# Optimization experiments

Measured on AMD Instinct MI355X. Metric: run time of the kernel, lower is better.

## Reference

```python
import jax, jax.numpy as jnp
import numpy as np

B, TK, H = 32, 1024, 512
N = 2 * H          # hidden_dim * 2
AD = 512           # attention_dimension


def setup_inputs() -> dict:
    key = jax.random.key(0)
    ks = jax.random.split(key, 11)
    s = 0.02  # weight scale
    return {
        's_t_hat': jax.random.normal(ks[0], (B, N), jnp.float32),
        'encoder_outputs': jax.random.normal(ks[1], (B, TK, N), jnp.float32),
        'encoder_feature': jax.random.normal(ks[2], (B * TK, N), jnp.float32),
        'enc_padding_mask': jax.random.uniform(ks[3], (B, TK), jnp.float32),
        'coverage': jax.random.uniform(ks[4], (B, TK), jnp.float32),
        'r_i': jax.random.normal(ks[5], (B, TK, AD), jnp.float32),
        'W_s_w': jax.random.normal(ks[6], (N, N), jnp.float32) * s,
        'W_s_b': jax.random.normal(ks[7], (N,), jnp.float32) * s,
        'W_c_w': jax.random.normal(ks[8], (N, 1), jnp.float32) * s,
        'v_w': jax.random.normal(ks[9], (1, N), jnp.float32) * s,
        'W_r_w': jax.random.normal(ks[10], (N, AD), jnp.float32) * s,
    }


def reference(s_t_hat, encoder_outputs, encoder_feature, enc_padding_mask,
              coverage, r_i, W_s_w, W_s_b, W_c_w, v_w, W_r_w):
    b, t_k, n = encoder_outputs.shape
    # decoder feature: W_s(s_t_hat), broadcast over time
    dec_fea = s_t_hat @ W_s_w.T + W_s_b                       # [b, n]
    enc_feat = encoder_feature.reshape(b, t_k, n)             # [b, t_k, n]
    # coverage feature: W_c applied to scalar coverage per position
    cov_feat = coverage[..., None] * W_c_w[:, 0]              # [b, t_k, n]
    e = jnp.tanh(enc_feat + dec_fea[:, None, :] + cov_feat)   # [b, t_k, n]
    scores = jnp.einsum('btn,n->bt', e, v_w[0])               # [b, t_k]
    attn_ = jax.nn.softmax(scores, axis=1) * enc_padding_mask
    attn = attn_ / attn_.sum(1, keepdims=True)                # renormalized
    c_t = jnp.einsum('bt,btn->bn', attn, encoder_outputs)     # [b, n]
    coverage_new = coverage + attn                            # [b, t_k]
    # structural (LSA) branch
    Wrri = jnp.einsum('bta,na->btn', r_i, W_r_w)              # [b, t_k, n]
    e_s = jnp.tanh(Wrri + dec_fea[:, None, :])
    s2 = jnp.einsum('btn,n->bt', e_s, v_w[0])
    a_struct = (jax.nn.softmax(s2, axis=1) * enc_padding_mask)[:, None, :]  # [b,1,t_k]
    c_t_struct = jnp.einsum('bt,btn->bn', a_struct[:, 0], encoder_outputs)  # [b, n]
    return (c_t, attn, coverage_new, c_t_struct, a_struct)
```

## Files before the change

### kernel.cpp

```cpp
#include <hip/hip_runtime.h>
#include <hip/hip_bf16.h>

static constexpr int BB   = 32;
static constexpr int TKK  = 1024;
static constexpr int ND   = 1024;
static constexpr int ADIM = 512;

typedef __attribute__((ext_vector_type(8))) short bf16x8;
typedef __attribute__((ext_vector_type(4))) float f32x4;

__device__ __forceinline__ float fast_tanh(float x) {
  x = fminf(fmaxf(x, -15.f), 15.f);
  float e = __expf(2.f * x);
  return __fdividef(e - 1.f, e + 1.f);
}

__device__ __forceinline__ short f2bf(float x) {
  unsigned u = __float_as_uint(x);
  u += 0x7FFF + ((u >> 16) & 1);
  return (short)(u >> 16);
}

__device__ __forceinline__ void gload_lds16(const void* g, void* l) {
  __builtin_amdgcn_global_load_lds(
      (const __attribute__((address_space(1))) unsigned int*)g,
      (__attribute__((address_space(3))) unsigned int*)l, 16, 0, 0);
}

__global__ __launch_bounds__(256) void k_cvt(const float* __restrict__ src,
    short* __restrict__ dst) {
  size_t i = (size_t)blockIdx.x * 256 + threadIdx.x;
  float4 a = ((const float4*)src)[2 * i];
  float4 b = ((const float4*)src)[2 * i + 1];
  bf16x8 h;
  h[0] = f2bf(a.x); h[1] = f2bf(a.y); h[2] = f2bf(a.z); h[3] = f2bf(a.w);
  h[4] = f2bf(b.x); h[5] = f2bf(b.y); h[6] = f2bf(b.z); h[7] = f2bf(b.w);
  ((bf16x8*)dst)[i] = h;
}

__global__ __launch_bounds__(256) void k_decfea(const float* __restrict__ s_t_hat,
    const float* __restrict__ Wsw, const float* __restrict__ Wsb,
    float* __restrict__ dec) {
  int b  = blockIdx.x >> 3;
  int n0 = (blockIdx.x & 7) << 7;
  int w = threadIdx.x >> 6, lane = threadIdx.x & 63;
  const float4* s4 = (const float4*)(s_t_hat + (size_t)b * ND);
  float4 sv0 = s4[lane], sv1 = s4[lane + 64], sv2 = s4[lane + 128], sv3 = s4[lane + 192];
  for (int nn = 0; nn < 32; nn++) {
    int n = n0 + w * 32 + nn;
    const float4* w4 = (const float4*)(Wsw + (size_t)n * ND);
    float4 wa = w4[lane], wb = w4[lane + 64], wc = w4[lane + 128], wd = w4[lane + 192];
    float acc = sv0.x*wa.x + sv0.y*wa.y + sv0.z*wa.z + sv0.w*wa.w
              + sv1.x*wb.x + sv1.y*wb.y + sv1.z*wb.z + sv1.w*wb.w
              + sv2.x*wc.x + sv2.y*wc.y + sv2.z*wc.z + sv2.w*wc.w
              + sv3.x*wd.x + sv3.y*wd.y + sv3.z*wd.z + sv3.w*wd.w;
    #pragma unroll
    for (int off = 32; off; off >>= 1) acc += __shfl_down(acc, off);
    if (lane == 0) dec[b * ND + n] = acc + Wsb[n];
  }
}

__global__ __launch_bounds__(256) void k_scoresA(const float* __restrict__ ef,
    const float* __restrict__ dec, const float* __restrict__ Wc,
    const float* __restrict__ vw, const float* __restrict__ cov,
    float* __restrict__ scores) {
  __shared__ float sb[4];
  int bt = blockIdx.x;
  int b  = bt >> 10;
  int tid = threadIdx.x;
  float4 e = *(const float4*)(ef + (size_t)bt * ND + tid * 4);
  float4 d = *(const float4*)(dec + (size_t)b * ND + tid * 4);
  float4 w = *(const float4*)(Wc + tid * 4);
  float4 v = *(const float4*)(vw + tid * 4);
  float c = cov[bt];
  float s = v.x * fast_tanh(e.x + d.x + c * w.x)
          + v.y * fast_tanh(e.y + d.y + c * w.y)
          + v.z * fast_tanh(e.z + d.z + c * w.z)
          + v.w * fast_tanh(e.w + d.w + c * w.w);
  #pragma unroll
  for (int off = 32; off; off >>= 1) s += __shfl_down(s, off);
  if ((tid & 63) == 0) sb[tid >> 6] = s;
  __syncthreads();
  if (tid == 0) scores[bt] = sb[0] + sb[1] + sb[2] + sb[3];
}

__global__ __launch_bounds__(256) void k_softmaxA(const float* __restrict__ scores,
    const float* __restrict__ mask, const float* __restrict__ cov,
    float* __restrict__ attn, float* __restrict__ covnew) {
  __shared__ float sb[4];
  int b = blockIdx.x, tid = threadIdx.x;
  float4 s = *(const float4*)(scores + (size_t)b * TKK + tid * 4);
  float m = fmaxf(fmaxf(s.x, s.y), fmaxf(s.z, s.w));
  #pragma unroll
  for (int off = 32; off; off >>= 1) m = fmaxf(m, __shfl_down(m, off));
  if ((tid & 63) == 0) sb[tid >> 6] = m;
  __syncthreads();
  m = fmaxf(fmaxf(sb[0], sb[1]), fmaxf(sb[2], sb[3]));
  float4 mk = *(const float4*)(mask + (size_t)b * TKK + tid * 4);
  float4 e;
  e.x = __expf(s.x - m) * mk.x;
  e.y = __expf(s.y - m) * mk.y;
  e.z = __expf(s.z - m) * mk.z;
  e.w = __expf(s.w - m) * mk.w;
  float sum = e.x + e.y + e.z + e.w;
  #pragma unroll
  for (int off = 32; off; off >>= 1) sum += __shfl_down(sum, off);
  __syncthreads();
  if ((tid & 63) == 0) sb[tid >> 6] = sum;
  __syncthreads();
  float inv = __fdividef(1.f, sb[0] + sb[1] + sb[2] + sb[3]);
  float4 a = {e.x * inv, e.y * inv, e.z * inv, e.w * inv};
  *(float4*)(attn + (size_t)b * TKK + tid * 4) = a;
  float4 c = *(const float4*)(cov + (size_t)b * TKK + tid * 4);
  float4 cn = {c.x + a.x, c.y + a.y, c.z + a.z, c.w + a.w};
  *(float4*)(covnew + (size_t)b * TKK + tid * 4) = cn;
}

__global__ __launch_bounds__(256) void k_gemmB3(const short* __restrict__ rb,
    const short* __restrict__ wb, const float* __restrict__ dec,
    const float* __restrict__ vw, float* __restrict__ part) {
  __shared__ __align__(16) short As[128 * 64];
  __shared__ __align__(16) short Bs[128 * 64];
  const int tid = threadIdx.x;
  const int lane = tid & 63, wv = tid >> 6;
  const int wm = wv >> 1, wn = wv & 1;
  const int g = lane >> 4, cl = lane & 15;
  const int mchunk = blockIdx.x, nchunk = blockIdx.y;
  const int b  = mchunk >> 3;
  const int t0 = (mchunk & 7) * 128;
  const int n0 = nchunk * 128;
  const int lrow = lane >> 3;
  const int lk   = (lane & 7) * 8;
  const short* Agbase = rb + (size_t)(b * TKK + t0) * ADIM;
  const short* Bgbase = wb + (size_t)n0 * ADIM;

  f32x4 acc[4][4];
  #pragma unroll
  for (int m = 0; m < 4; ++m)
    #pragma unroll
    for (int n = 0; n < 4; ++n) acc[m][n] = (f32x4){0.f, 0.f, 0.f, 0.f};

  for (int kc = 0; kc < 8; ++kc) {
    const int k0 = kc * 64;
    __syncthreads();
    #pragma unroll
    for (int i = 0; i < 4; ++i) {
      const int rowc = i * 32 + wv * 8;
      const int row  = rowc + lrow;
      gload_lds16(Agbase + (size_t)row * ADIM + k0 + lk, &As[rowc * 64]);
      gload_lds16(Bgbase + (size_t)row * ADIM + k0 + lk, &Bs[rowc * 64]);
    }
    __syncthreads();
    #pragma unroll
    for (int kf = 0; kf < 2; ++kf) {
      bf16x8 af[4], bfr[4];
      #pragma unroll
      for (int m = 0; m < 4; ++m)
        af[m] = *(const bf16x8*)&As[(wm * 64 + m * 16 + cl) * 64 + kf * 32 + g * 8];
      #pragma unroll
      for (int n = 0; n < 4; ++n)
        bfr[n] = *(const bf16x8*)&Bs[(wn * 64 + n * 16 + cl) * 64 + kf * 32 + g * 8];
      #pragma unroll
      for (int m = 0; m < 4; ++m)
        #pragma unroll
        for (int n = 0; n < 4; ++n)
          acc[m][n] = __builtin_amdgcn_mfma_f32_16x16x32_bf16(af[m], bfr[n], acc[m][n], 0, 0, 0);
    }
  }

  float vvv[4], ddd[4];
  #pragma unroll
  for (int n = 0; n < 4; ++n) {
    const int col = n0 + wn * 64 + n * 16 + cl;
    vvv[n] = vw[col];
    ddd[n] = dec[b * ND + col];
  }
  #pragma unroll
  for (int m = 0; m < 4; ++m) {
    #pragma unroll
    for (int r = 0; r < 4; ++r) {
      float s = 0.f;
      #pragma unroll
      for (int n = 0; n < 4; ++n)
        s += vvv[n] * fast_tanh(acc[m][n][r] + ddd[n]);
      #pragma unroll
      for (int off = 1; off < 16; off <<= 1) s += __shfl_xor(s, off);
      if (cl == 0) {
        const int rowg = b * TKK + t0 + wm * 64 + m * 16 + g * 4 + r;
        part[(size_t)rowg * 16 + nchunk * 2 + wn] = s;
      }
    }
  }
}

__global__ __launch_bounds__(256) void k_gemmB(const float* __restrict__ r_i,
    const float* __restrict__ Wr, const float* __restrict__ dec,
    const float* __restrict__ vw, float* __restrict__ part) {
  __shared__ short As[128 * 64];
  __shared__ short Bs[128 * 64];
  const int tid = threadIdx.x;
  const int lane = tid & 63, wv = tid >> 6;
  const int wm = wv >> 1, wn = wv & 1;
  const int g = lane >> 4, cl = lane & 15;
  const int mchunk = blockIdx.x, nchunk = blockIdx.y;
  const int b  = mchunk >> 3;
  const int t0 = (mchunk & 7) * 128;
  const int n0 = nchunk * 128;
  const float* Ag = r_i + (size_t)(b * TKK + t0) * ADIM;
  const float* Bg = Wr + (size_t)n0 * ADIM;
  const int srow = tid >> 3, skk = (tid & 7) * 8;

  f32x4 acc[4][4];
  #pragma unroll
  for (int m = 0; m < 4; ++m)
    #pragma unroll
    for (int n = 0; n < 4; ++n) acc[m][n] = (f32x4){0.f, 0.f, 0.f, 0.f};

  for (int kc = 0; kc < 8; ++kc) {
    const int k0 = kc * 64;
    __syncthreads();
    #pragma unroll
    for (int dit = 0; dit < 4; ++dit) {
      const int row = dit * 32 + srow;
      const float* sa = Ag + (size_t)row * ADIM + k0 + skk;
      float4 a0 = *(const float4*)sa, a1 = *(const float4*)(sa + 4);
      bf16x8 ha;
      ha[0]=f2bf(a0.x); ha[1]=f2bf(a0.y); ha[2]=f2bf(a0.z); ha[3]=f2bf(a0.w);
      ha[4]=f2bf(a1.x); ha[5]=f2bf(a1.y); ha[6]=f2bf(a1.z); ha[7]=f2bf(a1.w);
      *(bf16x8*)&As[row * 64 + skk] = ha;
      const float* sbp = Bg + (size_t)row * ADIM + k0 + skk;
      float4 b0 = *(const float4*)sbp, b1 = *(const float4*)(sbp + 4);
      bf16x8 hb;
      hb[0]=f2bf(b0.x); hb[1]=f2bf(b0.y); hb[2]=f2bf(b0.z); hb[3]=f2bf(b0.w);
      hb[4]=f2bf(b1.x); hb[5]=f2bf(b1.y); hb[6]=f2bf(b1.z); hb[7]=f2bf(b1.w);
      *(bf16x8*)&Bs[row * 64 + skk] = hb;
    }
    __syncthreads();
    #pragma unroll
    for (int kf = 0; kf < 2; ++kf) {
      bf16x8 af[4], bfr[4];
      #pragma unroll
      for (int m = 0; m < 4; ++m)
        af[m] = *(const bf16x8*)&As[(wm * 64 + m * 16 + cl) * 64 + kf * 32 + g * 8];
      #pragma unroll
      for (int n = 0; n < 4; ++n)
        bfr[n] = *(const bf16x8*)&Bs[(wn * 64 + n * 16 + cl) * 64 + kf * 32 + g * 8];
      #pragma unroll
      for (int m = 0; m < 4; ++m)
        #pragma unroll
        for (int n = 0; n < 4; ++n)
          acc[m][n] = __builtin_amdgcn_mfma_f32_16x16x32_bf16(af[m], bfr[n], acc[m][n], 0, 0, 0);
    }
  }
  float vvv[4], ddd[4];
  #pragma unroll
  for (int n = 0; n < 4; ++n) {
    const int col = n0 + wn * 64 + n * 16 + cl;
    vvv[n] = vw[col];
    ddd[n] = dec[b * ND + col];
  }
  #pragma unroll
  for (int m = 0; m < 4; ++m) {
    #pragma unroll
    for (int r = 0; r < 4; ++r) {
      float s = 0.f;
      #pragma unroll
      for (int n = 0; n < 4; ++n)
        s += vvv[n] * fast_tanh(acc[m][n][r] + ddd[n]);
      #pragma unroll
      for (int off = 1; off < 16; off <<= 1) s += __shfl_xor(s, off);
      if (cl == 0) {
        const int rowg = b * TKK + t0 + wm * 64 + m * 16 + g * 4 + r;
        part[(size_t)rowg * 16 + nchunk * 2 + wn] = s;
      }
    }
  }
}

__global__ __launch_bounds__(256) void k_softmaxB(const float* __restrict__ part,
    const float* __restrict__ mask, float* __restrict__ astruct) {
  __shared__ float sb[4];
  int b = blockIdx.x, tid = threadIdx.x;
  float sv[4];
  #pragma unroll
  for (int tt = 0; tt < 4; ++tt) {
    const float4* pp = (const float4*)(part + ((size_t)b * TKK + tid * 4 + tt) * 16);
    float4 q0 = pp[0], q1 = pp[1], q2 = pp[2], q3 = pp[3];
    sv[tt] = q0.x+q0.y+q0.z+q0.w + q1.x+q1.y+q1.z+q1.w
           + q2.x+q2.y+q2.z+q2.w + q3.x+q3.y+q3.z+q3.w;
  }
  float m = fmaxf(fmaxf(sv[0], sv[1]), fmaxf(sv[2], sv[3]));
  #pragma unroll
  for (int off = 32; off; off >>= 1) m = fmaxf(m, __shfl_down(m, off));
  if ((tid & 63) == 0) sb[tid >> 6] = m;
  __syncthreads();
  m = fmaxf(fmaxf(sb[0], sb[1]), fmaxf(sb[2], sb[3]));
  float e0 = __expf(sv[0] - m), e1 = __expf(sv[1] - m);
  float e2 = __expf(sv[2] - m), e3 = __expf(sv[3] - m);
  float sum = e0 + e1 + e2 + e3;
  #pragma unroll
  for (int off = 32; off; off >>= 1) sum += __shfl_down(sum, off);
  __syncthreads();
  if ((tid & 63) == 0) sb[tid >> 6] = sum;
  __syncthreads();
  float inv = __fdividef(1.f, sb[0] + sb[1] + sb[2] + sb[3]);
  float4 mk = *(const float4*)(mask + (size_t)b * TKK + tid * 4);
  float4 a = {e0 * mk.x * inv, e1 * mk.y * inv, e2 * mk.z * inv, e3 * mk.w * inv};
  *(float4*)(astruct + (size_t)b * TKK + tid * 4) = a;
}

__global__ __launch_bounds__(256) void k_ctx(const float* __restrict__ enc,
    const float* __restrict__ attn, const float* __restrict__ astr,
    float* __restrict__ partials) {
  int tc = blockIdx.x, b = blockIdx.y;
  int tid = threadIdx.x, lane = tid & 63;
  float a1v = attn[(size_t)b * TKK + tc * 64 + lane];
  float a2v = astr[(size_t)b * TKK + tc * 64 + lane];
  const float4* e4 = (const float4*)(enc + (size_t)(b * TKK + tc * 64) * ND);
  float4 ac = {0, 0, 0, 0}, as = {0, 0, 0, 0};
  #pragma unroll 4
  for (int m = 0; m < 64; m++) {
    float a1 = __shfl(a1v, m), a2 = __shfl(a2v, m);
    float4 ev = e4[(size_t)m * 256 + tid];
    ac.x += a1 * ev.x; ac.y += a1 * ev.y; ac.z += a1 * ev.z; ac.w += a1 * ev.w;
    as.x += a2 * ev.x; as.y += a2 * ev.y; as.z += a2 * ev.z; as.w += a2 * ev.w;
  }
  float* p = partials + (size_t)(b * 16 + tc) * 2 * ND;
  *(float4*)(p + tid * 4) = ac;
  *(float4*)(p + ND + tid * 4) = as;
}

__global__ __launch_bounds__(256) void k_reduce(const float* __restrict__ partials,
    float* __restrict__ ct, float* __restrict__ cts) {
  int b = blockIdx.x, tid = threadIdx.x;
  float4 sc = {0, 0, 0, 0}, ss = {0, 0, 0, 0};
  for (int tc = 0; tc < 16; tc++) {
    const float* p = partials + (size_t)(b * 16 + tc) * 2 * ND;
    float4 p1 = *(const float4*)(p + tid * 4);
    float4 p2 = *(const float4*)(p + ND + tid * 4);
    sc.x += p1.x; sc.y += p1.y; sc.z += p1.z; sc.w += p1.w;
    ss.x += p2.x; ss.y += p2.y; ss.z += p2.z; ss.w += p2.w;
  }
  *(float4*)(ct + (size_t)b * ND + tid * 4) = sc;
  *(float4*)(cts + (size_t)b * ND + tid * 4) = ss;
}

extern "C" void kernel_launch(void* const* d_in, const int* in_sizes, int n_in,
                              void* d_out, int out_size, void* d_ws, size_t ws_size,
                              hipStream_t stream) {
  const float* s_t_hat = (const float*)d_in[0];
  const float* enc_out  = (const float*)d_in[1];
  const float* enc_feat = (const float*)d_in[2];
  const float* mask     = (const float*)d_in[3];
  const float* cov      = (const float*)d_in[4];
  const float* r_i      = (const float*)d_in[5];
  const float* Wsw      = (const float*)d_in[6];
  const float* Wsb      = (const float*)d_in[7];
  const float* Wc       = (const float*)d_in[8];
  const float* vw       = (const float*)d_in[9];
  const float* Wr       = (const float*)d_in[10];

  float* out    = (float*)d_out;
  float* ct     = out;
  float* attn   = out + 32768;
  float* covnew = out + 65536;
  float* cts    = out + 98304;
  float* astr   = out + 131072;

  float* ws       = (float*)d_ws;
  float* dec      = ws;
  float* scores   = ws + 32768;
  float* s2part   = ws + 65536;
  float* partials = ws + 589824;
  short* rb       = (short*)(ws + 1638400);
  short* wb       = rb + 16777216;
  const size_t NEEDED = 1638400ull * 4 + 16777216ull * 2 + 524288ull * 2;

  k_decfea<<<256, 256, 0, stream>>>(s_t_hat, Wsw, Wsb, dec);
  k_scoresA<<<BB * TKK, 256, 0, stream>>>(enc_feat, dec, Wc, vw, cov, scores);
  k_softmaxA<<<BB, 256, 0, stream>>>(scores, mask, cov, attn, covnew);
  if (ws_size >= NEEDED) {
    k_cvt<<<8192, 256, 0, stream>>>(r_i, rb);
    k_cvt<<<256, 256, 0, stream>>>(Wr, wb);
    k_gemmB3<<<dim3(256, 8), 256, 0, stream>>>(rb, wb, dec, vw, s2part);
  } else {
    k_gemmB<<<dim3(256, 8), 256, 0, stream>>>(r_i, Wr, dec, vw, s2part);
  }
  k_softmaxB<<<BB, 256, 0, stream>>>(s2part, mask, astr);
  k_ctx<<<dim3(16, BB), 256, 0, stream>>>(enc_out, attn, astr, partials);
  k_reduce<<<BB, 256, 0, stream>>>(partials, ct, cts);
}
```

Baseline: 198.2 us.

## Double-buffer LDS tiles and XOR-swizzle layout in structural GEMM kernel

The r_i x W_r GEMM kernel now keeps two LDS buffers and issues the direct-to-LDS global loads for the next K chunk before running MFMAs on the current one. This overlaps global memory latency with compute and drops one barrier per iteration. The LDS layout is also XOR-swizzled by row so that the 16-byte fragment reads avoid bank conflicts. LDS use doubles, which can lower occupancy.

```diff
diff --git a/kernel.cpp b/kernel.cpp
--- a/kernel.cpp
+++ b/kernel.cpp
@@ -119,8 +119,8 @@
 __global__ __launch_bounds__(256) void k_gemmB3(const short* __restrict__ rb,
     const short* __restrict__ wb, const float* __restrict__ dec,
     const float* __restrict__ vw, float* __restrict__ part) {
-  __shared__ __align__(16) short As[128 * 64];
-  __shared__ __align__(16) short Bs[128 * 64];
+  __shared__ __align__(16) short As[2][128 * 64];
+  __shared__ __align__(16) short Bs[2][128 * 64];
   const int tid = threadIdx.x;
   const int lane = tid & 63, wv = tid >> 6;
   const int wm = wv >> 1, wn = wv & 1;
@@ -129,10 +129,11 @@
   const int b  = mchunk >> 3;
   const int t0 = (mchunk & 7) * 128;
   const int n0 = nchunk * 128;
-  const int lrow = lane >> 3;
-  const int lk   = (lane & 7) * 8;
+  const int srow8  = lane >> 3;
+  const int sk     = ((lane & 7) ^ srow8) * 8;
   const short* Agbase = rb + (size_t)(b * TKK + t0) * ADIM;
   const short* Bgbase = wb + (size_t)n0 * ADIM;
+  const int rsw = (cl & 7) << 3;
 
   f32x4 acc[4][4];
   #pragma unroll
@@ -140,32 +141,40 @@
     #pragma unroll
     for (int n = 0; n < 4; ++n) acc[m][n] = (f32x4){0.f, 0.f, 0.f, 0.f};
 
+  auto stage = [&](int buf, int kc) {
+    const int k0 = kc * 64;
+    #pragma unroll
+    for (int p = 0; p < 4; ++p) {
+      const int rowc = p * 32 + wv * 8;
+      const int row  = rowc + srow8;
+      gload_lds16(Agbase + (size_t)row * ADIM + k0 + sk, &As[buf][rowc * 64]);
+      gload_lds16(Bgbase + (size_t)row * ADIM + k0 + sk, &Bs[buf][rowc * 64]);
+    }
+  };
+
+  stage(0, 0);
+  __syncthreads();
   for (int kc = 0; kc < 8; ++kc) {
-    const int k0 = kc * 64;
-    __syncthreads();
-    #pragma unroll
-    for (int i = 0; i < 4; ++i) {
-      const int rowc = i * 32 + wv * 8;
-      const int row  = rowc + lrow;
-      gload_lds16(Agbase + (size_t)row * ADIM + k0 + lk, &As[rowc * 64]);
-      gload_lds16(Bgbase + (size_t)row * ADIM + k0 + lk, &Bs[rowc * 64]);
-    }
-    __syncthreads();
+    const int cur = kc & 1;
+    if (kc < 7) stage(cur ^ 1, kc + 1);
     #pragma unroll
     for (int kf = 0; kf < 2; ++kf) {
       bf16x8 af[4], bfr[4];
       #pragma unroll
       for (int m = 0; m < 4; ++m)
-        af[m] = *(const bf16x8*)&As[(wm * 64 + m * 16 + cl) * 64 + kf * 32 + g * 8];
+        af[m] = *(const bf16x8*)&As[cur][(wm * 64 + m * 16 + cl) * 64
+                                         + (((kf * 4 + g) * 8) ^ rsw)];
       #pragma unroll
       for (int n = 0; n < 4; ++n)
-        bfr[n] = *(const bf16x8*)&Bs[(wn * 64 + n * 16 + cl) * 64 + kf * 32 + g * 8];
+        bfr[n] = *(const bf16x8*)&Bs[cur][(wn * 64 + n * 16 + cl) * 64
+                                          + (((kf * 4 + g) * 8) ^ rsw)];
       #pragma unroll
       for (int m = 0; m < 4; ++m)
         #pragma unroll
         for (int n = 0; n < 4; ++n)
           acc[m][n] = __builtin_amdgcn_mfma_f32_16x16x32_bf16(af[m], bfr[n], acc[m][n], 0, 0, 0);
     }
+    __syncthreads();
   }
 
   float vvv[4], ddd[4];
```

New measurement: 185.2 us. 1.07x faster.
